# Kernel tuning notes

Measured on AMD Instinct MI355X. Metric: run time of the kernel, lower is better.

Reference implementation:

```python
import jax, jax.numpy as jnp
import numpy as np

N, NC, E = 100000, 50000, 1600000   # source points, centers, edges
D, P, H, O = 64, 3, 128, 128        # feat dim, pos dim, hidden, out


def setup_inputs() -> dict:
    key = jax.random.key(0)
    ks = jax.random.split(key, 10)
    x = jax.random.normal(ks[0], (N, D), jnp.float32)
    x_c = jax.random.normal(ks[1], (NC, O), jnp.float32)  # only shape is used
    pos = jax.random.normal(ks[2], (N, P), jnp.float32)
    pos_c = jax.random.normal(ks[3], (NC, P), jnp.float32)
    src = jax.random.randint(ks[4], (E,), 0, N)
    dst = jax.random.randint(ks[5], (E,), 0, NC)
    W1 = jax.random.normal(ks[6], (D + P, H), jnp.float32) / jnp.sqrt(D + P)
    b1 = jnp.zeros((H,), jnp.float32)
    W2 = jax.random.normal(ks[7], (H, O), jnp.float32) / jnp.sqrt(H)
    b2 = jnp.zeros((O,), jnp.float32)
    return dict(x=x, x_c=x_c, pos=pos, pos_c=pos_c, src=src, dst=dst,
                W1=W1, b1=b1, W2=W2, b2=b2)


def reference(x, x_c, pos, pos_c, src, dst, W1, b1, W2, b2):
    # gather per-edge features: [E, D+P]
    feats = jnp.concatenate([x[src], pos[src] - pos_c[dst]], axis=1)
    # MLP on edges
    h = jax.nn.relu(feats @ W1 + b1) @ W2 + b2  # [E, O]
    # scatter-max aggregation onto centers
    agg = jax.ops.segment_max(h, dst, num_segments=x_c.shape[0])  # [NC, O]
    # match torch_scatter convention: empty segments -> 0 (not -inf)
    return jnp.where(jnp.isneginf(agg), 0.0, agg)
```

## Files before the change

### kernel.cpp

```cpp
#include <hip/hip_runtime.h>
#include <hip/hip_bf16.h>

#define NPTS   100000
#define NCENT  50000
#define NEDGE  1600000
#define DF     64
#define DP     3
#define DH     128
#define DOUT   128
#define TILE   128
#define LDA    104
#define LDH    136
#define LDF    66
#define NCPAD  50176

typedef __attribute__((ext_vector_type(8))) short short8;
typedef __attribute__((ext_vector_type(4))) float f32x4;

__device__ __forceinline__ unsigned short f2bf(float f) {
  union { __hip_bfloat16 h; unsigned short u; } v;
  v.h = __float2bfloat16(f);
  return v.u;
}

__device__ __forceinline__ unsigned encodeKey(float f) {
  unsigned u = __float_as_uint(f);
  return u ^ ((unsigned)((int)u >> 31) | 0x80000000u);
}

__device__ __forceinline__ float decodeKey(unsigned k) {
  if (k == 0u) return 0.0f;
  unsigned u = (k & 0x80000000u) ? (k ^ 0x80000000u) : ~k;
  return __uint_as_float(u);
}


__global__ void k_zero(int* __restrict__ cnt) {
  cnt[blockIdx.x * 256 + threadIdx.x] = 0;
}

__global__ void k_rank(const int* __restrict__ dst, int* __restrict__ cnt,
                       int* __restrict__ rank) {
  int i = blockIdx.x * 256 + threadIdx.x;
  rank[i] = atomicAdd(&cnt[dst[i]], 1);
}

__global__ void k_s1(const int* __restrict__ cnt, int* __restrict__ bsum) {
  __shared__ int sh[256];
  int t = threadIdx.x;
  sh[t] = cnt[blockIdx.x * 256 + t];
  __syncthreads();
  for (int off = 128; off > 0; off >>= 1) {
    if (t < off) sh[t] += sh[t + off];
    __syncthreads();
  }
  if (t == 0) bsum[blockIdx.x] = sh[0];
}

__global__ void k_s2(const int* __restrict__ bsum, int* __restrict__ bbase) {
  __shared__ int sh[256];
  int t = threadIdx.x;
  int v = (t < 196) ? bsum[t] : 0;
  sh[t] = v;
  __syncthreads();
  for (int off = 1; off < 256; off <<= 1) {
    int u = (t >= off) ? sh[t - off] : 0;
    __syncthreads();
    sh[t] += u;
    __syncthreads();
  }
  if (t < 196) bbase[t] = sh[t] - v;
}

__global__ void k_s3(int* __restrict__ cnt, const int* __restrict__ bbase) {
  __shared__ int sh[256];
  int t = threadIdx.x, i = blockIdx.x * 256 + t;
  int v = cnt[i];
  sh[t] = v;
  __syncthreads();
  for (int off = 1; off < 256; off <<= 1) {
    int u = (t >= off) ? sh[t - off] : 0;
    __syncthreads();
    sh[t] += u;
    __syncthreads();
  }
  cnt[i] = sh[t] - v + bbase[blockIdx.x];
}

__global__ void k_place(const int* __restrict__ src, const int* __restrict__ dst,
                        const int* __restrict__ base, const int* __restrict__ rank,
                        int* __restrict__ srcS, int* __restrict__ dstS) {
  int i = blockIdx.x * 256 + threadIdx.x;
  int d = dst[i];
  int p = base[d] + rank[i];
  srcS[p] = src[i];
  dstS[p] = d;
}


__global__ void k_pack_w1(const float* __restrict__ W1, unsigned short* __restrict__ W1f) {
  int tid = blockIdx.x * blockDim.x + threadIdx.x;
  int lane = tid & 63, g = tid >> 6;
  int nt = g / 3, ks = g % 3;
  int n = nt * 16 + (lane & 15);
  int k0 = ks * 32 + (lane >> 4) * 8;
  short8 v;
  for (int j = 0; j < 8; ++j) {
    int k = k0 + j;
    float f = (k < DF + DP) ? W1[k * DH + n] : 0.0f;
    v[j] = (short)f2bf(f);
  }
  *reinterpret_cast<short8*>(W1f + (size_t)tid * 8) = v;
}

__global__ void k_pack_w2(const float* __restrict__ W2, unsigned short* __restrict__ W2f) {
  int tid = blockIdx.x * blockDim.x + threadIdx.x;
  int lane = tid & 63, g = tid >> 6;
  int nt = g >> 2, ks = g & 3;
  int n = nt * 16 + (lane & 15);
  int k0 = ks * 32 + (lane >> 4) * 8;
  short8 v;
  for (int j = 0; j < 8; ++j) {
    int k = k0 + j;
    v[j] = (short)f2bf(W2[k * DH + n]);
  }
  *reinterpret_cast<short8*>(W2f + (size_t)tid * 8) = v;
}

__global__ void k_init(unsigned* __restrict__ out) {
  int i = blockIdx.x * blockDim.x + threadIdx.x;
  reinterpret_cast<uint4*>(out)[i] = make_uint4(0u, 0u, 0u, 0u);
}

__global__ void k_decode(unsigned* __restrict__ out) {
  int i = blockIdx.x * blockDim.x + threadIdx.x;
  uint4 v = reinterpret_cast<uint4*>(out)[i];
  float4 f;
  f.x = decodeKey(v.x);
  f.y = decodeKey(v.y);
  f.z = decodeKey(v.z);
  f.w = decodeKey(v.w);
  reinterpret_cast<float4*>(out)[i] = f;
}

__global__ void __launch_bounds__(256, 4)
k_mlp(const float* __restrict__ x, const float* __restrict__ pos,
      const float* __restrict__ pos_c, const int* __restrict__ srcS,
      const int* __restrict__ dstS, const float* __restrict__ b1,
      const float* __restrict__ b2, const unsigned short* __restrict__ W1f,
      const unsigned short* __restrict__ W2f, unsigned* __restrict__ outU) {
  __shared__ __align__(16) unsigned short buf[TILE * LDH];
  __shared__ int dstLoc[TILE];

  const int t = threadIdx.x;
  const int e0 = blockIdx.x * TILE;

  {
    const int e = t >> 1, p = t & 1;
    const int s = srcS[e0 + e];
    const float4* xr = reinterpret_cast<const float4*>(x + (size_t)s * DF);
    for (int i = 0; i < 4; ++i) {
      float4 v0 = xr[p * 8 + 2 * i];
      float4 v1 = xr[p * 8 + 2 * i + 1];
      short8 w;
      w[0] = (short)f2bf(v0.x); w[1] = (short)f2bf(v0.y);
      w[2] = (short)f2bf(v0.z); w[3] = (short)f2bf(v0.w);
      w[4] = (short)f2bf(v1.x); w[5] = (short)f2bf(v1.y);
      w[6] = (short)f2bf(v1.z); w[7] = (short)f2bf(v1.w);
      *reinterpret_cast<short8*>(&buf[e * LDA + p * 32 + i * 8]) = w;
    }
    short8 z = {0, 0, 0, 0, 0, 0, 0, 0};
    *reinterpret_cast<short8*>(&buf[e * LDA + 72 + p * 16]) = z;
    *reinterpret_cast<short8*>(&buf[e * LDA + 72 + p * 16 + 8]) = z;
  }
  if (t < TILE) {
    const int s = srcS[e0 + t];
    const int c = dstS[e0 + t];
    dstLoc[t] = c;
    float dx = pos[(size_t)s * 3 + 0] - pos_c[(size_t)c * 3 + 0];
    float dy = pos[(size_t)s * 3 + 1] - pos_c[(size_t)c * 3 + 1];
    float dz = pos[(size_t)s * 3 + 2] - pos_c[(size_t)c * 3 + 2];
    short8 w = {0, 0, 0, 0, 0, 0, 0, 0};
    w[0] = (short)f2bf(dx); w[1] = (short)f2bf(dy); w[2] = (short)f2bf(dz);
    *reinterpret_cast<short8*>(&buf[t * LDA + 64]) = w;
  }
  __syncthreads();

  const int lane = t & 63;
  const int w = t >> 6;
  const int l16 = lane & 15;
  const int quad = lane >> 4;

  short8 a1[2][3];
  for (int mi = 0; mi < 2; ++mi) {
    int row = (2 * w + mi) * 16 + l16;
    for (int ks = 0; ks < 3; ++ks)
      a1[mi][ks] = *reinterpret_cast<const short8*>(&buf[row * LDA + ks * 32 + quad * 8]);
  }
  __syncthreads();

  for (int nt = 0; nt < 8; ++nt) {
    short8 b[3];
    for (int ks = 0; ks < 3; ++ks)
      b[ks] = *reinterpret_cast<const short8*>(W1f + ((size_t)(nt * 3 + ks) * 64 + lane) * 8);
    f32x4 acc0 = {0.f, 0.f, 0.f, 0.f}, acc1 = {0.f, 0.f, 0.f, 0.f};
    for (int ks = 0; ks < 3; ++ks) {
      acc0 = __builtin_amdgcn_mfma_f32_16x16x32_bf16(a1[0][ks], b[ks], acc0, 0, 0, 0);
      acc1 = __builtin_amdgcn_mfma_f32_16x16x32_bf16(a1[1][ks], b[ks], acc1, 0, 0, 0);
    }
    int n = nt * 16 + l16;
    float bias = b1[n];
    for (int r = 0; r < 4; ++r) {
      float v0 = acc0[r] + bias; v0 = v0 > 0.f ? v0 : 0.f;
      buf[((2 * w) * 16 + quad * 4 + r) * LDH + n] = f2bf(v0);
      float v1 = acc1[r] + bias; v1 = v1 > 0.f ? v1 : 0.f;
      buf[((2 * w + 1) * 16 + quad * 4 + r) * LDH + n] = f2bf(v1);
    }
  }
  __syncthreads();

  short8 a2[2][4];
  for (int mi = 0; mi < 2; ++mi) {
    int row = (2 * w + mi) * 16 + l16;
    for (int ks = 0; ks < 4; ++ks)
      a2[mi][ks] = *reinterpret_cast<const short8*>(&buf[row * LDH + ks * 32 + quad * 8]);
  }
  __syncthreads();

  float* Sf = reinterpret_cast<float*>(buf);
  const int col = t & 63;
  const int chunk = t >> 6;

  for (int half = 0; half < 2; ++half) {
    for (int ntl = 0; ntl < 4; ++ntl) {
      const int nt = half * 4 + ntl;
      short8 b[4];
      for (int ks = 0; ks < 4; ++ks)
        b[ks] = *reinterpret_cast<const short8*>(W2f + ((size_t)(nt * 4 + ks) * 64 + lane) * 8);
      f32x4 acc0 = {0.f, 0.f, 0.f, 0.f}, acc1 = {0.f, 0.f, 0.f, 0.f};
      for (int ks = 0; ks < 4; ++ks) {
        acc0 = __builtin_amdgcn_mfma_f32_16x16x32_bf16(a2[0][ks], b[ks], acc0, 0, 0, 0);
        acc1 = __builtin_amdgcn_mfma_f32_16x16x32_bf16(a2[1][ks], b[ks], acc1, 0, 0, 0);
      }
      const int nl = ntl * 16 + l16;
      const float bias = b2[half * 64 + nl];
      for (int r = 0; r < 4; ++r) {
        int edge0 = (2 * w) * 16 + quad * 4 + r;
        Sf[edge0 * LDF + nl] = acc0[r] + bias;
        int edge1 = (2 * w + 1) * 16 + quad * 4 + r;
        Sf[edge1 * LDF + nl] = acc1[r] + bias;
      }
    }
    __syncthreads();
    float running = -3.402823466e38f;
    int cur_d = dstLoc[chunk * 32];
    for (int i = 0; i < 32; ++i) {
      const int ei = chunk * 32 + i;
      const int d = dstLoc[ei];
      if (d != cur_d) {
        atomicMax(&outU[(size_t)cur_d * DOUT + half * 64 + col], encodeKey(running));
        running = -3.402823466e38f;
        cur_d = d;
      }
      running = fmaxf(running, Sf[ei * LDF + col]);
    }
    atomicMax(&outU[(size_t)cur_d * DOUT + half * 64 + col], encodeKey(running));
    __syncthreads();
  }
}

extern "C" void kernel_launch(void* const* d_in, const int* in_sizes, int n_in,
                              void* d_out, int out_size, void* d_ws, size_t ws_size,
                              hipStream_t stream) {
  const float* x     = (const float*)d_in[0];
  const float* pos   = (const float*)d_in[2];
  const float* pos_c = (const float*)d_in[3];
  const int*   src   = (const int*)d_in[4];
  const int*   dst   = (const int*)d_in[5];
  const float* W1    = (const float*)d_in[6];
  const float* b1    = (const float*)d_in[7];
  const float* W2    = (const float*)d_in[8];
  const float* b2    = (const float*)d_in[9];
  unsigned* outU = (unsigned*)d_out;

  char* base = (char*)d_ws;
  unsigned short* W1f = (unsigned short*)base;
  unsigned short* W2f = (unsigned short*)(base + 24576);
  int* cnt   = (int*)(base + 65536);
  int* bsum  = (int*)(base + 65536 + 200704);
  int* bbase = (int*)(base + 65536 + 200704 + 1024);
  int* rank  = (int*)(base + 65536 + 200704 + 2048);
  int* srcS  = (int*)(base + 65536 + 200704 + 2048 + 6400000);
  int* dstS  = (int*)(base + 65536 + 200704 + 2048 + 12800000);

  k_zero<<<NCPAD / 256, 256, 0, stream>>>(cnt);
  k_rank<<<NEDGE / 256, 256, 0, stream>>>(dst, cnt, rank);
  k_s1<<<NCPAD / 256, 256, 0, stream>>>(cnt, bsum);
  k_s2<<<1, 256, 0, stream>>>(bsum, bbase);
  k_s3<<<NCPAD / 256, 256, 0, stream>>>(cnt, bbase);
  k_place<<<NEDGE / 256, 256, 0, stream>>>(src, dst, cnt, rank, srcS, dstS);
  k_pack_w1<<<6, 256, 0, stream>>>(W1, W1f);
  k_pack_w2<<<8, 256, 0, stream>>>(W2, W2f);
  k_init<<<(NCENT * DOUT / 4) / 256, 256, 0, stream>>>(outU);
  k_mlp<<<NEDGE / TILE, 256, 0, stream>>>(x, pos, pos_c, srcS, dstS,
                                          b1, b2, W1f, W2f, outU);
  k_decode<<<(NCENT * DOUT / 4) / 256, 256, 0, stream>>>(outU);
}
```

Before: 430.6 us.

## Pre-convert x to bf16, pack src/dst into 64-bit records, fuse prep kernels

Adds a single prep kernel that zeroes the output and counts, converts x to bf16 once, and packs W1/W2, replacing four separate launches. The edge sort now writes one 64-bit (dst,src) record instead of two int arrays, so the MLP kernel reads a single word per edge. The MLP gather then loads 128-byte bf16 rows instead of 256-byte fp32 rows and drops per-edge conversion work. The cost is an extra full pass over x (read fp32, write bf16) and more workspace memory.

Measured after the change: 396.7 us. -7.9%, faster.

```diff
diff --git a/kernel.cpp b/kernel.cpp
--- a/kernel.cpp
+++ b/kernel.cpp
@@ -34,10 +34,55 @@
   return __uint_as_float(u);
 }
 
-
-__global__ void k_zero(int* __restrict__ cnt) {
-  cnt[blockIdx.x * 256 + threadIdx.x] = 0;
-}
+__global__ void k_prep(const float* __restrict__ x, const float* __restrict__ W1,
+                       const float* __restrict__ W2, unsigned short* __restrict__ xbf,
+                       unsigned short* __restrict__ W1f, unsigned short* __restrict__ W2f,
+                       int* __restrict__ cnt, unsigned* __restrict__ outU) {
+  const int b = blockIdx.x;
+  const int t = threadIdx.x;
+  if (b < 6250) {
+    int i = b * 256 + t;
+    reinterpret_cast<uint4*>(outU)[i] = make_uint4(0u, 0u, 0u, 0u);
+  } else if (b < 9375) {
+    int i = (b - 6250) * 256 + t;
+    const float4* xr = reinterpret_cast<const float4*>(x);
+    float4 v0 = xr[2 * i], v1 = xr[2 * i + 1];
+    short8 w;
+    w[0] = (short)f2bf(v0.x); w[1] = (short)f2bf(v0.y);
+    w[2] = (short)f2bf(v0.z); w[3] = (short)f2bf(v0.w);
+    w[4] = (short)f2bf(v1.x); w[5] = (short)f2bf(v1.y);
+    w[6] = (short)f2bf(v1.z); w[7] = (short)f2bf(v1.w);
+    reinterpret_cast<short8*>(xbf)[i] = w;
+  } else if (b < 9571) {
+    cnt[(b - 9375) * 256 + t] = 0;
+  } else if (b < 9577) {
+    int tid = (b - 9571) * 256 + t;
+    int lane = tid & 63, g = tid >> 6;
+    int nt = g / 3, ks = g % 3;
+    int n = nt * 16 + (lane & 15);
+    int k0 = ks * 32 + (lane >> 4) * 8;
+    short8 v;
+    for (int j = 0; j < 8; ++j) {
+      int k = k0 + j;
+      float f = (k < DF + DP) ? W1[k * DH + n] : 0.0f;
+      v[j] = (short)f2bf(f);
+    }
+    *reinterpret_cast<short8*>(W1f + (size_t)tid * 8) = v;
+  } else {
+    int tid = (b - 9577) * 256 + t;
+    int lane = tid & 63, g = tid >> 6;
+    int nt = g >> 2, ks = g & 3;
+    int n = nt * 16 + (lane & 15);
+    int k0 = ks * 32 + (lane >> 4) * 8;
+    short8 v;
+    for (int j = 0; j < 8; ++j) {
+      int k = k0 + j;
+      v[j] = (short)f2bf(W2[k * DH + n]);
+    }
+    *reinterpret_cast<short8*>(W2f + (size_t)tid * 8) = v;
+  }
+}
+
 
 __global__ void k_rank(const int* __restrict__ dst, int* __restrict__ cnt,
                        int* __restrict__ rank) {
@@ -89,47 +134,11 @@
 
 __global__ void k_place(const int* __restrict__ src, const int* __restrict__ dst,
                         const int* __restrict__ base, const int* __restrict__ rank,
-                        int* __restrict__ srcS, int* __restrict__ dstS) {
+                        unsigned long long* __restrict__ sdS) {
   int i = blockIdx.x * 256 + threadIdx.x;
   int d = dst[i];
   int p = base[d] + rank[i];
-  srcS[p] = src[i];
-  dstS[p] = d;
-}
-
-
-__global__ void k_pack_w1(const float* __restrict__ W1, unsigned short* __restrict__ W1f) {
-  int tid = blockIdx.x * blockDim.x + threadIdx.x;
-  int lane = tid & 63, g = tid >> 6;
-  int nt = g / 3, ks = g % 3;
-  int n = nt * 16 + (lane & 15);
-  int k0 = ks * 32 + (lane >> 4) * 8;
-  short8 v;
-  for (int j = 0; j < 8; ++j) {
-    int k = k0 + j;
-    float f = (k < DF + DP) ? W1[k * DH + n] : 0.0f;
-    v[j] = (short)f2bf(f);
-  }
-  *reinterpret_cast<short8*>(W1f + (size_t)tid * 8) = v;
-}
-
-__global__ void k_pack_w2(const float* __restrict__ W2, unsigned short* __restrict__ W2f) {
-  int tid = blockIdx.x * blockDim.x + threadIdx.x;
-  int lane = tid & 63, g = tid >> 6;
-  int nt = g >> 2, ks = g & 3;
-  int n = nt * 16 + (lane & 15);
-  int k0 = ks * 32 + (lane >> 4) * 8;
-  short8 v;
-  for (int j = 0; j < 8; ++j) {
-    int k = k0 + j;
-    v[j] = (short)f2bf(W2[k * DH + n]);
-  }
-  *reinterpret_cast<short8*>(W2f + (size_t)tid * 8) = v;
-}
-
-__global__ void k_init(unsigned* __restrict__ out) {
-  int i = blockIdx.x * blockDim.x + threadIdx.x;
-  reinterpret_cast<uint4*>(out)[i] = make_uint4(0u, 0u, 0u, 0u);
+  sdS[p] = ((unsigned long long)(unsigned)d << 32) | (unsigned)src[i];
 }
 
 __global__ void k_decode(unsigned* __restrict__ out) {
@@ -144,11 +153,11 @@
 }
 
 __global__ void __launch_bounds__(256, 4)
-k_mlp(const float* __restrict__ x, const float* __restrict__ pos,
-      const float* __restrict__ pos_c, const int* __restrict__ srcS,
-      const int* __restrict__ dstS, const float* __restrict__ b1,
-      const float* __restrict__ b2, const unsigned short* __restrict__ W1f,
-      const unsigned short* __restrict__ W2f, unsigned* __restrict__ outU) {
+k_mlp(const unsigned short* __restrict__ xbf, const float* __restrict__ pos,
+      const float* __restrict__ pos_c, const unsigned long long* __restrict__ sdS,
+      const float* __restrict__ b1, const float* __restrict__ b2,
+      const unsigned short* __restrict__ W1f, const unsigned short* __restrict__ W2f,
+      unsigned* __restrict__ outU) {
   __shared__ __align__(16) unsigned short buf[TILE * LDH];
   __shared__ int dstLoc[TILE];
 
@@ -157,25 +166,19 @@
 
   {
     const int e = t >> 1, p = t & 1;
-    const int s = srcS[e0 + e];
-    const float4* xr = reinterpret_cast<const float4*>(x + (size_t)s * DF);
-    for (int i = 0; i < 4; ++i) {
-      float4 v0 = xr[p * 8 + 2 * i];
-      float4 v1 = xr[p * 8 + 2 * i + 1];
-      short8 w;
-      w[0] = (short)f2bf(v0.x); w[1] = (short)f2bf(v0.y);
-      w[2] = (short)f2bf(v0.z); w[3] = (short)f2bf(v0.w);
-      w[4] = (short)f2bf(v1.x); w[5] = (short)f2bf(v1.y);
-      w[6] = (short)f2bf(v1.z); w[7] = (short)f2bf(v1.w);
-      *reinterpret_cast<short8*>(&buf[e * LDA + p * 32 + i * 8]) = w;
-    }
+    const unsigned long long rec = sdS[e0 + e];
+    const int s = (int)(rec & 0xffffffffu);
+    const short8* xr = reinterpret_cast<const short8*>(xbf + (size_t)s * DF);
+    for (int i = 0; i < 4; ++i)
+      *reinterpret_cast<short8*>(&buf[e * LDA + p * 32 + i * 8]) = xr[p * 4 + i];
     short8 z = {0, 0, 0, 0, 0, 0, 0, 0};
     *reinterpret_cast<short8*>(&buf[e * LDA + 72 + p * 16]) = z;
     *reinterpret_cast<short8*>(&buf[e * LDA + 72 + p * 16 + 8]) = z;
   }
   if (t < TILE) {
-    const int s = srcS[e0 + t];
-    const int c = dstS[e0 + t];
+    const unsigned long long rec = sdS[e0 + t];
+    const int s = (int)(rec & 0xffffffffu);
+    const int c = (int)(rec >> 32);
     dstLoc[t] = c;
     float dx = pos[(size_t)s * 3 + 0] - pos_c[(size_t)c * 3 + 0];
     float dy = pos[(size_t)s * 3 + 1] - pos_c[(size_t)c * 3 + 1];
@@ -286,23 +289,20 @@
   char* base = (char*)d_ws;
   unsigned short* W1f = (unsigned short*)base;
   unsigned short* W2f = (unsigned short*)(base + 24576);
+  int* bsum  = (int*)(base + 57344);
+  int* bbase = (int*)(base + 58368);
   int* cnt   = (int*)(base + 65536);
-  int* bsum  = (int*)(base + 65536 + 200704);
-  int* bbase = (int*)(base + 65536 + 200704 + 1024);
-  int* rank  = (int*)(base + 65536 + 200704 + 2048);
-  int* srcS  = (int*)(base + 65536 + 200704 + 2048 + 6400000);
-  int* dstS  = (int*)(base + 65536 + 200704 + 2048 + 12800000);
-
-  k_zero<<<NCPAD / 256, 256, 0, stream>>>(cnt);
+  int* rank  = (int*)(base + 266240);
+  unsigned long long* sdS = (unsigned long long*)(base + 6666240);
+  unsigned short* xbf = (unsigned short*)(base + 19466240);
+
+  k_prep<<<9585, 256, 0, stream>>>(x, W1, W2, xbf, W1f, W2f, cnt, outU);
   k_rank<<<NEDGE / 256, 256, 0, stream>>>(dst, cnt, rank);
   k_s1<<<NCPAD / 256, 256, 0, stream>>>(cnt, bsum);
   k_s2<<<1, 256, 0, stream>>>(bsum, bbase);
   k_s3<<<NCPAD / 256, 256, 0, stream>>>(cnt, bbase);
-  k_place<<<NEDGE / 256, 256, 0, stream>>>(src, dst, cnt, rank, srcS, dstS);
-  k_pack_w1<<<6, 256, 0, stream>>>(W1, W1f);
-  k_pack_w2<<<8, 256, 0, stream>>>(W2, W2f);
-  k_init<<<(NCENT * DOUT / 4) / 256, 256, 0, stream>>>(outU);
-  k_mlp<<<NEDGE / TILE, 256, 0, stream>>>(x, pos, pos_c, srcS, dstS,
+  k_place<<<NEDGE / 256, 256, 0, stream>>>(src, dst, cnt, rank, sdS);
+  k_mlp<<<NEDGE / TILE, 256, 0, stream>>>(xbf, pos, pos_c, sdS,
                                           b1, b2, W1f, W2f, outU);
   k_decode<<<(NCENT * DOUT / 4) / 256, 256, 0, stream>>>(outU);
 }
```
